# Kernel tuning notes

Hardware: AMD Instinct MI355X
Metric: run time of the kernel (lower is better)

## Reference

```python
import jax, jax.numpy as jnp
import numpy as np

SEQ_LEN, BATCH, INPUT, HIDDEN, N_OUT = 512, 128, 512, 1024, 4


def setup_inputs() -> dict:
    key = jax.random.key(0)
    ks = jax.random.split(key, 8)
    s_ih = 1.0 / np.sqrt(HIDDEN)
    inp = {
        "inputs": jax.random.normal(ks[0], (SEQ_LEN, BATCH, INPUT), dtype=jnp.float32),
        "h0": jnp.zeros((BATCH, HIDDEN), dtype=jnp.float32),
        "c0": jnp.zeros((BATCH, HIDDEN), dtype=jnp.float32),
        # PyTorch LSTMCell params: weight_ih [4H, I], weight_hh [4H, H], biases [4H]
        "W_ih": jax.random.uniform(ks[1], (4 * HIDDEN, INPUT), jnp.float32, -s_ih, s_ih),
        "W_hh": jax.random.uniform(ks[2], (4 * HIDDEN, HIDDEN), jnp.float32, -s_ih, s_ih),
        "b_ih": jax.random.uniform(ks[3], (4 * HIDDEN,), jnp.float32, -s_ih, s_ih),
        "b_hh": jax.random.uniform(ks[4], (4 * HIDDEN,), jnp.float32, -s_ih, s_ih),
        "W_dec": jax.random.uniform(ks[5], (N_OUT, HIDDEN), jnp.float32, -s_ih, s_ih),
        "b_dec": jax.random.uniform(ks[6], (N_OUT,), jnp.float32, -s_ih, s_ih),
    }
    return inp


def reference(inputs, h0, c0, W_ih, W_hh, b_ih, b_hh, W_dec, b_dec):
    # Precompute input projections for all timesteps in one big GEMM:
    # [S, B, I] @ [I, 4H] -> [S, B, 4H]
    x_proj = jnp.einsum('sbi,gi->sbg', inputs, W_ih) + b_ih + b_hh

    def step(carry, xp):
        h, c = carry
        gates = xp + h @ W_hh.T  # [B, 4H]
        i, f, g, o = jnp.split(gates, 4, axis=-1)  # PyTorch gate order i,f,g,o
        i = jax.nn.sigmoid(i)
        f = jax.nn.sigmoid(f)
        g = jnp.tanh(g)
        o = jax.nn.sigmoid(o)
        c_new = f * c + i * g
        h_new = o * jnp.tanh(c_new)
        return (h_new, c_new), None

    (h_last, _), _ = jax.lax.scan(step, (h0, c0), x_proj)
    logits = h_last @ W_dec.T + b_dec  # [B, 4]
    # Original applies nn.Softmax(dim=0), i.e. over the batch dimension.
    return jax.nn.softmax(logits, axis=0)
```

## Files before the change

### kernel.cpp

```cpp
#include <hip/hip_runtime.h>
#include <math.h>

#define SEQ   512
#define BATCH 128
#define INP   512
#define HID   1024
#define G4    4096
#define NOUT  4

typedef short bf16x8 __attribute__((ext_vector_type(8)));
typedef float f32x4  __attribute__((ext_vector_type(4)));

__device__ __forceinline__ unsigned short f2bf(float x) {
  unsigned int u = __float_as_uint(x);
  unsigned int r = (u + 0x7FFFu + ((u >> 16) & 1u)) >> 16;
  return (unsigned short)r;
}
__device__ __forceinline__ float bf2f(unsigned short h) {
  return __uint_as_float(((unsigned int)h) << 16);
}

__global__ void prepack_w(const float* __restrict__ W,
                          unsigned short* __restrict__ Whi,
                          unsigned short* __restrict__ Wlo) {
  int T = blockIdx.x * blockDim.x + threadIdx.x;
  int L = T & 63;
  int kstep = (T >> 6) & 31;
  int bk = T >> 11;
  int m = L & 15, q = L >> 4;
  int row = (m & 3) * HID + bk * 4 + (m >> 2);
  int k = kstep * 32 + q * 8;
  const float* src = W + (size_t)row * HID + k;
  unsigned short hi[8], lo[8];
#pragma unroll
  for (int i = 0; i < 8; i++) {
    float x = src[i];
    unsigned short h = f2bf(x);
    hi[i] = h;
    lo[i] = f2bf(x - bf2f(h));
  }
  size_t o = (size_t)T * 8;
#pragma unroll
  for (int i = 0; i < 8; i++) { Whi[o + i] = hi[i]; Wlo[o + i] = lo[i]; }
}

__global__ void init_state(const float* __restrict__ h0, const float* __restrict__ c0,
                           unsigned short* __restrict__ hhi, unsigned short* __restrict__ hlo,
                           float* __restrict__ cT) {
  int idx = blockIdx.x * blockDim.x + threadIdx.x;
  int b = idx >> 10;
  int j = idx & (HID - 1);
  float x = h0[idx];
  unsigned short h = f2bf(x);
  hhi[idx] = h;
  hlo[idx] = f2bf(x - bf2f(h));
  cT[j * BATCH + b] = c0[idx];
}

__global__ void transpose_in(const float* __restrict__ in, float* __restrict__ xt,
                             int nrows) {
  __shared__ float s[32][33];
  int tx = threadIdx.x & 31, ty = threadIdx.x >> 5;
  int n0 = blockIdx.x * 32, i0 = blockIdx.y * 32;
#pragma unroll
  for (int r = 0; r < 4; r++) {
    int n = n0 + ty + 8 * r;
    s[ty + 8 * r][tx] = in[(size_t)n * INP + i0 + tx];
  }
  __syncthreads();
#pragma unroll
  for (int r = 0; r < 4; r++) {
    int i = i0 + ty + 8 * r;
    xt[(size_t)i * nrows + n0 + tx] = s[tx][ty + 8 * r];
  }
}

__global__ __launch_bounds__(256, 3)
void gemm_xproj(const float* __restrict__ A, const float* __restrict__ Bm,
                const float* __restrict__ b_ih, const float* __restrict__ b_hh,
                float* __restrict__ C, int N) {
  __shared__ float As[32][128];
  __shared__ float Bs[32][128];
  int t = threadIdx.x;
  int g0 = blockIdx.x * 128;
  int n0 = blockIdx.y * 128;
  int mg = (t >> 4) * 8, nn = (t & 15) * 8;
  float acc[8][8] = {};
  for (int k0 = 0; k0 < INP; k0 += 32) {
#pragma unroll
    for (int r = 0; r < 4; r++) {
      int idx = t + 256 * r;
      int g = idx >> 3, i4 = idx & 7;
      float4 v = *(const float4*)&A[(size_t)(g0 + g) * INP + k0 + 4 * i4];
      As[4 * i4 + 0][g] = v.x; As[4 * i4 + 1][g] = v.y;
      As[4 * i4 + 2][g] = v.z; As[4 * i4 + 3][g] = v.w;
    }
#pragma unroll
    for (int r = 0; r < 4; r++) {
      int idx = t + 256 * r;
      int kk = idx >> 5, n4 = idx & 31;
      *(float4*)&Bs[kk][4 * n4] = *(const float4*)&Bm[(size_t)(k0 + kk) * N + n0 + 4 * n4];
    }
    __syncthreads();
#pragma unroll 4
    for (int kk = 0; kk < 32; kk++) {
      float4 a0 = *(const float4*)&As[kk][mg];
      float4 a1 = *(const float4*)&As[kk][mg + 4];
      float4 bb0 = *(const float4*)&Bs[kk][nn];
      float4 bb1 = *(const float4*)&Bs[kk][nn + 4];
      float av[8] = {a0.x, a0.y, a0.z, a0.w, a1.x, a1.y, a1.z, a1.w};
      float bv[8] = {bb0.x, bb0.y, bb0.z, bb0.w, bb1.x, bb1.y, bb1.z, bb1.w};
#pragma unroll
      for (int i2 = 0; i2 < 8; i2++)
#pragma unroll
        for (int j2 = 0; j2 < 8; j2++)
          acc[i2][j2] = fmaf(av[i2], bv[j2], acc[i2][j2]);
    }
    __syncthreads();
  }
#pragma unroll
  for (int i2 = 0; i2 < 8; i2++) {
    int g = g0 + mg + i2;
    float bias = b_ih[g] + b_hh[g];
#pragma unroll
    for (int j2 = 0; j2 < 8; j2++) {
      C[(size_t)g * N + n0 + nn + j2] = acc[i2][j2] + bias;
    }
  }
}

__global__ __launch_bounds__(512)
void lstm_step(const unsigned short* __restrict__ Whi,
               const unsigned short* __restrict__ Wlo,
               const float* __restrict__ xp, int N,
               const unsigned short* __restrict__ hin_hi,
               const unsigned short* __restrict__ hin_lo,
               unsigned short* __restrict__ hout_hi,
               unsigned short* __restrict__ hout_lo,
               float* __restrict__ cT) {
  __shared__ bf16x8 Wlds[4096];

  int bk = blockIdx.x;
  int t = threadIdx.x;
  int w = t >> 6;
  int L = t & 63;
  int n = L & 15, q = L >> 4;

  {
    float4* ldsf = (float4*)Wlds;
    const float4* s1 = (const float4*)(Whi + (size_t)bk * 16384);
    const float4* s2 = (const float4*)(Wlo + (size_t)bk * 16384);
#pragma unroll
    for (int i = 0; i < 4; i++) ldsf[t + 512 * i] = s1[t + 512 * i];
#pragma unroll
    for (int i = 0; i < 4; i++) ldsf[2048 + t + 512 * i] = s2[t + 512 * i];
  }

  int j = bk * 4 + q;
  int b = w * 16 + n;
  int ci = j * BATCH + b;
  float xpv[4];
#pragma unroll
  for (int g = 0; g < 4; g++)
    xpv[g] = xp[(size_t)(g * HID + j) * N + b];
  float cold = cT[ci];

  __syncthreads();

  const unsigned short* Bh = hin_hi + (size_t)b * HID + q * 8;
  const unsigned short* Bl = hin_lo + (size_t)b * HID + q * 8;

  f32x4 acc = {0.f, 0.f, 0.f, 0.f};
#pragma unroll 4
  for (int ks = 0; ks < 32; ks++) {
    bf16x8 ah = Wlds[ks * 64 + L];
    bf16x8 al = Wlds[2048 + ks * 64 + L];
    bf16x8 bh = *(const bf16x8*)(Bh + ks * 32);
    bf16x8 bl = *(const bf16x8*)(Bl + ks * 32);
    acc = __builtin_amdgcn_mfma_f32_16x16x32_bf16(ah, bh, acc, 0, 0, 0);
    acc = __builtin_amdgcn_mfma_f32_16x16x32_bf16(ah, bl, acc, 0, 0, 0);
    acc = __builtin_amdgcn_mfma_f32_16x16x32_bf16(al, bh, acc, 0, 0, 0);
  }

  float pre[4];
#pragma unroll
  for (int g = 0; g < 4; g++)
    pre[g] = acc[g] + xpv[g];

  float ig = 1.f / (1.f + expf(-pre[0]));
  float fg = 1.f / (1.f + expf(-pre[1]));
  float gg = tanhf(pre[2]);
  float og = 1.f / (1.f + expf(-pre[3]));
  float cn = fg * cold + ig * gg;
  cT[ci] = cn;
  float hn = og * tanhf(cn);

  unsigned short hh = f2bf(hn);
  hout_hi[(size_t)b * HID + j] = hh;
  hout_lo[(size_t)b * HID + j] = f2bf(hn - bf2f(hh));
}

__global__ void decode_softmax(const unsigned short* __restrict__ hhi,
                               const unsigned short* __restrict__ hlo,
                               const float* __restrict__ Wd,
                               const float* __restrict__ bd, float* __restrict__ out) {
  __shared__ float lg[NOUT][BATCH];
  __shared__ float mx[NOUT], sm[NOUT];
  int t = threadIdx.x;
  int b = t >> 2, o = t & 3;
  float s = bd[o];
  for (int j = 0; j < HID; j++) {
    float hv = bf2f(hhi[(size_t)b * HID + j]) + bf2f(hlo[(size_t)b * HID + j]);
    s += hv * Wd[o * HID + j];
  }
  lg[o][b] = s;
  __syncthreads();
  if (t < NOUT) {
    float m = -1e30f;
    for (int b2 = 0; b2 < BATCH; b2++) m = fmaxf(m, lg[t][b2]);
    float ss = 0.f;
    for (int b2 = 0; b2 < BATCH; b2++) ss += expf(lg[t][b2] - m);
    mx[t] = m; sm[t] = ss;
  }
  __syncthreads();
  out[b * NOUT + o] = expf(lg[o][b] - mx[o]) / sm[o];
}

extern "C" void kernel_launch(void* const* d_in, const int* in_sizes, int n_in,
                              void* d_out, int out_size, void* d_ws, size_t ws_size,
                              hipStream_t stream) {
  const float* inputs = (const float*)d_in[0];
  const float* h0     = (const float*)d_in[1];
  const float* c0     = (const float*)d_in[2];
  const float* W_ih   = (const float*)d_in[3];
  const float* W_hh   = (const float*)d_in[4];
  const float* b_ih   = (const float*)d_in[5];
  const float* b_hh   = (const float*)d_in[6];
  const float* W_dec  = (const float*)d_in[7];
  const float* b_dec  = (const float*)d_in[8];
  float* out = (float*)d_out;

  char* w = (char*)d_ws;
  unsigned short* Whi = (unsigned short*)w;  w += (size_t)G4 * HID * 2;
  unsigned short* Wlo = (unsigned short*)w;  w += (size_t)G4 * HID * 2;
  unsigned short* hhi[2], *hlo[2];
  hhi[0] = (unsigned short*)w;  w += (size_t)BATCH * HID * 2;
  hhi[1] = (unsigned short*)w;  w += (size_t)BATCH * HID * 2;
  hlo[0] = (unsigned short*)w;  w += (size_t)BATCH * HID * 2;
  hlo[1] = (unsigned short*)w;  w += (size_t)BATCH * HID * 2;
  float* cT = (float*)w;        w += (size_t)HID * BATCH * 4;
  size_t used = (size_t)(w - (char*)d_ws);

  size_t per_ct = ((size_t)INP * BATCH + (size_t)G4 * BATCH) * 4;
  int CT = 1;
  if (ws_size > used) {
    size_t avail = (ws_size - used) / per_ct;
    for (int c = SEQ; c >= 1; c >>= 1)
      if ((size_t)c <= avail) { CT = c; break; }
  }
  float* Xt = (float*)w;  w += (size_t)INP * BATCH * CT * 4;
  float* XP = (float*)w;
  int N = CT * BATCH;

  prepack_w<<<(256 * 32 * 64) / 256, 256, 0, stream>>>(W_hh, Whi, Wlo);
  init_state<<<BATCH * HID / 256, 256, 0, stream>>>(h0, c0, hhi[0], hlo[0], cT);

  for (int t0 = 0; t0 < SEQ; t0 += CT) {
    transpose_in<<<dim3(N / 32, INP / 32), 256, 0, stream>>>(
        inputs + (size_t)t0 * BATCH * INP, Xt, N);
    gemm_xproj<<<dim3(G4 / 128, N / 128), 256, 0, stream>>>(
        W_ih, Xt, b_ih, b_hh, XP, N);
    for (int tt = 0; tt < CT; tt++) {
      int gs = t0 + tt;
      int src = gs & 1, dst = 1 - src;
      const float* xpc = XP + (size_t)tt * BATCH;
      lstm_step<<<256, 512, 0, stream>>>(
          Whi, Wlo, xpc, N, hhi[src], hlo[src], hhi[dst], hlo[dst], cT);
    }
  }

  decode_softmax<<<1, 512, 0, stream>>>(hhi[0], hlo[0], W_dec, b_dec, out);
}
```

Before: 13.29 ms.

## Replace per-step LSTM launches with persistent cooperative kernel using grid sync

Replaces the per-timestep lstm_step launches with one cooperative persistent kernel that loops over all timesteps in a chunk, keeping W_hh slices resident in LDS and the cell state in registers. Timesteps are separated by grid.sync instead of kernel boundaries. Each block now handles 8 hidden units for half the batch, reusing the loaded h fragments across two MFMA accumulators. This removes launch overhead and the repeated reload of W_hh into LDS every step. In exchange it pays grid-wide barrier latency, needs all 256 blocks co-resident, and uses 128KB of LDS per block.

```diff
diff --git a/kernel.cpp b/kernel.cpp
--- a/kernel.cpp
+++ b/kernel.cpp
@@ -1,5 +1,8 @@
 #include <hip/hip_runtime.h>
+#include <hip/hip_cooperative_groups.h>
 #include <math.h>
+
+namespace cg = cooperative_groups;
 
 #define SEQ   512
 #define BATCH 128
@@ -129,75 +132,111 @@
   }
 }
 
-__global__ __launch_bounds__(512)
-void lstm_step(const unsigned short* __restrict__ Whi,
-               const unsigned short* __restrict__ Wlo,
-               const float* __restrict__ xp, int N,
-               const unsigned short* __restrict__ hin_hi,
-               const unsigned short* __restrict__ hin_lo,
-               unsigned short* __restrict__ hout_hi,
-               unsigned short* __restrict__ hout_lo,
-               float* __restrict__ cT) {
-  __shared__ bf16x8 Wlds[4096];
+__global__ __launch_bounds__(256)
+void lstm_seq(const unsigned short* __restrict__ Whi,
+              const unsigned short* __restrict__ Wlo,
+              const float* __restrict__ XP, int N, int CT, int step0,
+              unsigned short* __restrict__ h0hi, unsigned short* __restrict__ h0lo,
+              unsigned short* __restrict__ h1hi, unsigned short* __restrict__ h1lo,
+              float* __restrict__ cT) {
+  __shared__ bf16x8 Wlds[8192];
+
+  cg::grid_group grid = cg::this_grid();
 
   int bk = blockIdx.x;
+  int jblk = bk >> 1;
+  int bh2 = bk & 1;
   int t = threadIdx.x;
   int w = t >> 6;
   int L = t & 63;
   int n = L & 15, q = L >> 4;
+  int b = bh2 * 64 + w * 16 + n;
+  int j0 = jblk * 8 + q;
 
   {
     float4* ldsf = (float4*)Wlds;
-    const float4* s1 = (const float4*)(Whi + (size_t)bk * 16384);
-    const float4* s2 = (const float4*)(Wlo + (size_t)bk * 16384);
-#pragma unroll
-    for (int i = 0; i < 4; i++) ldsf[t + 512 * i] = s1[t + 512 * i];
-#pragma unroll
-    for (int i = 0; i < 4; i++) ldsf[2048 + t + 512 * i] = s2[t + 512 * i];
-  }
-
-  int j = bk * 4 + q;
-  int b = w * 16 + n;
-  int ci = j * BATCH + b;
-  float xpv[4];
-#pragma unroll
-  for (int g = 0; g < 4; g++)
-    xpv[g] = xp[(size_t)(g * HID + j) * N + b];
-  float cold = cT[ci];
+    const float4* s1 = (const float4*)(Whi + (size_t)jblk * 32768);
+    const float4* s2 = (const float4*)(Wlo + (size_t)jblk * 32768);
+#pragma unroll
+    for (int i = 0; i < 16; i++) ldsf[t + 256 * i] = s1[t + 256 * i];
+#pragma unroll
+    for (int i = 0; i < 16; i++) ldsf[4096 + t + 256 * i] = s2[t + 256 * i];
+  }
+
+  int ci0 = j0 * BATCH + b;
+  int ci1 = (j0 + 4) * BATCH + b;
+  float cc0 = cT[ci0];
+  float cc1 = cT[ci1];
+
+  size_t hoff = (size_t)b * HID + q * 8;
+  size_t o0 = (size_t)b * HID + j0;
 
   __syncthreads();
 
-  const unsigned short* Bh = hin_hi + (size_t)b * HID + q * 8;
-  const unsigned short* Bl = hin_lo + (size_t)b * HID + q * 8;
-
-  f32x4 acc = {0.f, 0.f, 0.f, 0.f};
+  for (int tt = 0; tt < CT; tt++) {
+    int gs = step0 + tt;
+    int odd = gs & 1;
+    const unsigned short* Bh = (odd ? h1hi : h0hi) + hoff;
+    const unsigned short* Bl = (odd ? h1lo : h0lo) + hoff;
+    unsigned short* dhi = odd ? h0hi : h1hi;
+    unsigned short* dlo = odd ? h0lo : h1lo;
+    const float* xpc = XP + (size_t)tt * BATCH;
+
+    float xpv0[4], xpv1[4];
+#pragma unroll
+    for (int g = 0; g < 4; g++) {
+      xpv0[g] = xpc[(size_t)(g * HID + j0) * N + b];
+      xpv1[g] = xpc[(size_t)(g * HID + j0 + 4) * N + b];
+    }
+
+    f32x4 acc0 = {0.f, 0.f, 0.f, 0.f};
+    f32x4 acc1 = {0.f, 0.f, 0.f, 0.f};
 #pragma unroll 4
-  for (int ks = 0; ks < 32; ks++) {
-    bf16x8 ah = Wlds[ks * 64 + L];
-    bf16x8 al = Wlds[2048 + ks * 64 + L];
-    bf16x8 bh = *(const bf16x8*)(Bh + ks * 32);
-    bf16x8 bl = *(const bf16x8*)(Bl + ks * 32);
-    acc = __builtin_amdgcn_mfma_f32_16x16x32_bf16(ah, bh, acc, 0, 0, 0);
-    acc = __builtin_amdgcn_mfma_f32_16x16x32_bf16(ah, bl, acc, 0, 0, 0);
-    acc = __builtin_amdgcn_mfma_f32_16x16x32_bf16(al, bh, acc, 0, 0, 0);
-  }
-
-  float pre[4];
-#pragma unroll
-  for (int g = 0; g < 4; g++)
-    pre[g] = acc[g] + xpv[g];
-
-  float ig = 1.f / (1.f + expf(-pre[0]));
-  float fg = 1.f / (1.f + expf(-pre[1]));
-  float gg = tanhf(pre[2]);
-  float og = 1.f / (1.f + expf(-pre[3]));
-  float cn = fg * cold + ig * gg;
-  cT[ci] = cn;
-  float hn = og * tanhf(cn);
-
-  unsigned short hh = f2bf(hn);
-  hout_hi[(size_t)b * HID + j] = hh;
-  hout_lo[(size_t)b * HID + j] = f2bf(hn - bf2f(hh));
+    for (int ks = 0; ks < 32; ks++) {
+      bf16x8 bhv = *(const bf16x8*)(Bh + ks * 32);
+      bf16x8 blv = *(const bf16x8*)(Bl + ks * 32);
+      bf16x8 ah0 = Wlds[ks * 64 + L];
+      bf16x8 ah1 = Wlds[2048 + ks * 64 + L];
+      bf16x8 al0 = Wlds[4096 + ks * 64 + L];
+      bf16x8 al1 = Wlds[6144 + ks * 64 + L];
+      acc0 = __builtin_amdgcn_mfma_f32_16x16x32_bf16(ah0, bhv, acc0, 0, 0, 0);
+      acc1 = __builtin_amdgcn_mfma_f32_16x16x32_bf16(ah1, bhv, acc1, 0, 0, 0);
+      acc0 = __builtin_amdgcn_mfma_f32_16x16x32_bf16(ah0, blv, acc0, 0, 0, 0);
+      acc1 = __builtin_amdgcn_mfma_f32_16x16x32_bf16(ah1, blv, acc1, 0, 0, 0);
+      acc0 = __builtin_amdgcn_mfma_f32_16x16x32_bf16(al0, bhv, acc0, 0, 0, 0);
+      acc1 = __builtin_amdgcn_mfma_f32_16x16x32_bf16(al1, bhv, acc1, 0, 0, 0);
+    }
+
+    {
+      float i_ = 1.f / (1.f + expf(-(acc0[0] + xpv0[0])));
+      float f_ = 1.f / (1.f + expf(-(acc0[1] + xpv0[1])));
+      float g_ = tanhf(acc0[2] + xpv0[2]);
+      float o_ = 1.f / (1.f + expf(-(acc0[3] + xpv0[3])));
+      cc0 = f_ * cc0 + i_ * g_;
+      float hn = o_ * tanhf(cc0);
+      unsigned short hh = f2bf(hn);
+      dhi[o0] = hh;
+      dlo[o0] = f2bf(hn - bf2f(hh));
+    }
+    {
+      float i_ = 1.f / (1.f + expf(-(acc1[0] + xpv1[0])));
+      float f_ = 1.f / (1.f + expf(-(acc1[1] + xpv1[1])));
+      float g_ = tanhf(acc1[2] + xpv1[2]);
+      float o_ = 1.f / (1.f + expf(-(acc1[3] + xpv1[3])));
+      cc1 = f_ * cc1 + i_ * g_;
+      float hn = o_ * tanhf(cc1);
+      unsigned short hh = f2bf(hn);
+      dhi[o0 + 4] = hh;
+      dlo[o0 + 4] = f2bf(hn - bf2f(hh));
+    }
+
+    __threadfence();
+    grid.sync();
+    __threadfence();
+  }
+
+  cT[ci0] = cc0;
+  cT[ci1] = cc1;
 }
 
 __global__ void decode_softmax(const unsigned short* __restrict__ hhi,
@@ -270,13 +309,14 @@
         inputs + (size_t)t0 * BATCH * INP, Xt, N);
     gemm_xproj<<<dim3(G4 / 128, N / 128), 256, 0, stream>>>(
         W_ih, Xt, b_ih, b_hh, XP, N);
-    for (int tt = 0; tt < CT; tt++) {
-      int gs = t0 + tt;
-      int src = gs & 1, dst = 1 - src;
-      const float* xpc = XP + (size_t)tt * BATCH;
-      lstm_step<<<256, 512, 0, stream>>>(
-          Whi, Wlo, xpc, N, hhi[src], hlo[src], hhi[dst], hlo[dst], cT);
-    }
+
+    int Nv = N, CTv = CT, step0 = t0;
+    void* kargs[] = {
+        (void*)&Whi, (void*)&Wlo, (void*)&XP, (void*)&Nv, (void*)&CTv,
+        (void*)&step0, (void*)&hhi[0], (void*)&hlo[0], (void*)&hhi[1],
+        (void*)&hlo[1], (void*)&cT};
+    hipLaunchCooperativeKernel((const void*)lstm_seq, dim3(256), dim3(256),
+                               kargs, 0, stream);
   }
 
   decode_softmax<<<1, 512, 0, stream>>>(hhi[0], hlo[0], W_dec, b_dec, out);
```

Result: slower. 46.89 ms (+252.9%).
